# Optimization experiments

Hardware: AMD Instinct MI355X
Metric: run time of the kernel (lower is better)

## Reference

```python
import jax, jax.numpy as jnp
import numpy as np

N_NODES = 50000
N_EDGES = 1000000
D = 64          # input feature dim
H = 64          # hidden dim per conv layer / pooling out dim
N_GRAPHS = 256  # number of graphs in the batch


def setup_inputs() -> dict:
    key = jax.random.key(0)
    ks = jax.random.split(key, 10)
    x = jax.random.normal(ks[0], (N_NODES, D), dtype=jnp.float32)
    edge_index = jax.random.randint(ks[1], (2, N_EDGES), 0, N_NODES, dtype=jnp.int64)
    batch = jnp.sort(jax.random.randint(ks[2], (N_NODES,), 0, N_GRAPHS, dtype=jnp.int64))
    scale_in = 1.0 / np.sqrt(D)
    scale_h = 1.0 / np.sqrt(H)
    W1 = jax.random.normal(ks[3], (D, H), dtype=jnp.float32) * scale_in
    W2 = jax.random.normal(ks[4], (H, H), dtype=jnp.float32) * scale_h
    W3 = jax.random.normal(ks[5], (H, H), dtype=jnp.float32) * scale_h
    Wp1 = jax.random.normal(ks[6], (H, H), dtype=jnp.float32) * scale_h
    Wp2 = jax.random.normal(ks[7], (H, H), dtype=jnp.float32) * scale_h
    Wp3 = jax.random.normal(ks[8], (H, H), dtype=jnp.float32) * scale_h
    return {"x": x, "edge_index": edge_index, "batch": batch,
            "W1": W1, "W2": W2, "W3": W3,
            "Wp1": Wp1, "Wp2": Wp2, "Wp3": Wp3}


def _gcn_conv(x, W, src, dst):
    # PyG GCNConv with normalize=False, bias=False:
    #   h = x @ W; out[i] = sum_{(j->i) in E} h[j]   (no self-loops, unit edge weight)
    h = x @ W                                   # [N, H]
    return jax.ops.segment_sum(h[src], dst, num_segments=N_NODES)  # [N, H]


def reference(x, edge_index, batch, W1, W2, W3, Wp1, Wp2, Wp3):
    src, dst = edge_index[0], edge_index[1]
    x1 = jax.nn.relu(_gcn_conv(x, W1, src, dst))    # layer 0 output
    x2 = jax.nn.relu(_gcn_conv(x1, W2, src, dst))   # layer 1 output
    x3 = jax.nn.relu(_gcn_conv(x2, W3, src, dst))   # layer 2 output
    # Pooling: global_add_pool per layer output -> per-layer Linear -> stack -> sum -> relu
    p1 = jax.ops.segment_sum(x1, batch, num_segments=N_GRAPHS) @ Wp1  # [G, H]
    p2 = jax.ops.segment_sum(x2, batch, num_segments=N_GRAPHS) @ Wp2
    p3 = jax.ops.segment_sum(x3, batch, num_segments=N_GRAPHS) @ Wp3
    return jax.nn.relu(p1 + p2 + p3)                # [G, H]
```

## Files before the change

kernel.cpp:

```cpp
#include <hip/hip_runtime.h>
#include <hip/hip_bf16.h>

#define NN 50000
#define NE 1000000
#define DIM 64
#define NG 256
#define NBUCK 196
#define ROUND 4096
#define NBLK 245
#define TOT2D (NBUCK * NBLK)
#define SCANB 47

__global__ __launch_bounds__(512) void hist2d_kernel(const int* __restrict__ dst,
                                                     int* __restrict__ hist) {
    __shared__ int h[NBUCK];
    int t = threadIdx.x;
    if (t < NBUCK) h[t] = 0;
    __syncthreads();
    int base = blockIdx.x * ROUND;
#pragma unroll
    for (int it = 0; it < 8; ++it) {
        int e = base + it * 512 + t;
        if (e < NE) atomicAdd(&h[dst[e] >> 8], 1);
    }
    __syncthreads();
    if (t < NBUCK) hist[t * NBLK + blockIdx.x] = h[t];
}

__global__ __launch_bounds__(1024) void scanA_kernel(const int* __restrict__ hist,
                                                     int* __restrict__ blocksum) {
    __shared__ int tmp[1024];
    int t = threadIdx.x;
    int i = blockIdx.x * 1024 + t;
    tmp[t] = (i < TOT2D) ? hist[i] : 0;
    __syncthreads();
    for (int s = 512; s > 0; s >>= 1) {
        if (t < s) tmp[t] += tmp[t + s];
        __syncthreads();
    }
    if (t == 0) blocksum[blockIdx.x] = tmp[0];
}

__global__ __launch_bounds__(64) void scanB_kernel(int* __restrict__ blocksum) {
    __shared__ int tmp[64];
    int t = threadIdx.x;
    int v = (t < SCANB) ? blocksum[t] : 0;
    tmp[t] = v;
    __syncthreads();
    for (int off = 1; off < 64; off <<= 1) {
        int a = (t >= off) ? tmp[t - off] : 0;
        __syncthreads();
        tmp[t] += a;
        __syncthreads();
    }
    if (t < SCANB) blocksum[t] = tmp[t] - v;
}

__global__ __launch_bounds__(1024) void scanC_kernel(const int* __restrict__ hist,
                                                     const int* __restrict__ blocksum,
                                                     int* __restrict__ scanned) {
    __shared__ int tmp[1024];
    int t = threadIdx.x;
    int i = blockIdx.x * 1024 + t;
    int v = (i < TOT2D) ? hist[i] : 0;
    tmp[t] = v;
    __syncthreads();
    for (int off = 1; off < 1024; off <<= 1) {
        int a = (t >= off) ? tmp[t - off] : 0;
        __syncthreads();
        tmp[t] += a;
        __syncthreads();
    }
    if (i < TOT2D) scanned[i] = tmp[t] - v + blocksum[blockIdx.x];
}

__global__ __launch_bounds__(512) void permute_kernel(
    const int* __restrict__ src, const int* __restrict__ dst,
    const int* __restrict__ scanned, unsigned int* __restrict__ bucketed) {
    __shared__ int cur[NBUCK];
    int t = threadIdx.x;
    int blk = blockIdx.x;
    if (t < NBUCK) cur[t] = scanned[t * NBLK + blk];
    __syncthreads();
    int base = blk * ROUND;
#pragma unroll
    for (int it = 0; it < 8; ++it) {
        int e = base + it * 512 + t;
        if (e < NE) {
            int d = dst[e];
            int s = src[e];
            int b = d >> 8;
            int pos = atomicAdd(&cur[b], 1);
            bucketed[pos] = ((unsigned int)(d & 255) << 16) | (unsigned int)s;
        }
    }
}

__global__ __launch_bounds__(512) void bucket_sort_kernel(
    const unsigned int* __restrict__ bucketed, const int* __restrict__ scanned,
    int* __restrict__ offsets, int* __restrict__ csr) {
    __shared__ int hist[256];
    __shared__ int sc[256];
    __shared__ int cur[256];
    int b = blockIdx.x;
    int t = threadIdx.x;
    if (t < 256) hist[t] = 0;
    __syncthreads();
    int gbase = scanned[b * NBLK];
    int gend  = (b < NBUCK - 1) ? scanned[(b + 1) * NBLK] : NE;
    int count = gend - gbase;
    const unsigned int* bd = bucketed + gbase;
    for (int e = t; e < count; e += 512) atomicAdd(&hist[bd[e] >> 16], 1);
    __syncthreads();
    if (t < 256) sc[t] = hist[t];
    __syncthreads();
    for (int off = 1; off < 256; off <<= 1) {
        int a = 0;
        if (t < 256 && t >= off) a = sc[t - off];
        __syncthreads();
        if (t < 256) sc[t] += a;
        __syncthreads();
    }
    if (t < 256) {
        int excl = sc[t] - hist[t];
        cur[t] = excl;
        int node = b * 256 + t;
        if (node < NN) offsets[node] = gbase + excl;
    }
    if (b == NBUCK - 1 && t == 0) offsets[NN] = NE;
    __syncthreads();
    for (int e = t; e < count; e += 512) {
        unsigned int v = bd[e];
        int p = atomicAdd(&cur[v >> 16], 1);
        csr[gbase + p] = (int)(v & 0xFFFFu);
    }
}

__global__ __launch_bounds__(128) void gemm64_kernel(const float* __restrict__ X,
                                                     const float* __restrict__ W,
                                                     float* __restrict__ H, int nrows) {
    __shared__ float Xl[128 * 65];
    int t = threadIdx.x;
    int base = blockIdx.x * 128;
    for (int idx = t; idx < 128 * 16; idx += 128) {
        int row = idx >> 4;
        int c4  = idx & 15;
        float4 v = make_float4(0.f, 0.f, 0.f, 0.f);
        if (base + row < nrows)
            v = *reinterpret_cast<const float4*>(&X[(size_t)(base + row) * 64 + c4 * 4]);
        float* p = &Xl[row * 65 + c4 * 4];
        p[0] = v.x; p[1] = v.y; p[2] = v.z; p[3] = v.w;
    }
    __syncthreads();
    float acc[64];
#pragma unroll
    for (int c = 0; c < 64; ++c) acc[c] = 0.f;
#pragma unroll 4
    for (int k = 0; k < 64; ++k) {
        float xv = Xl[t * 65 + k];
#pragma unroll
        for (int c4 = 0; c4 < 16; ++c4) {
            float4 w = *reinterpret_cast<const float4*>(&W[k * 64 + c4 * 4]);
            acc[c4 * 4 + 0] = fmaf(xv, w.x, acc[c4 * 4 + 0]);
            acc[c4 * 4 + 1] = fmaf(xv, w.y, acc[c4 * 4 + 1]);
            acc[c4 * 4 + 2] = fmaf(xv, w.z, acc[c4 * 4 + 2]);
            acc[c4 * 4 + 3] = fmaf(xv, w.w, acc[c4 * 4 + 3]);
        }
    }
    int row = base + t;
    if (row < nrows) {
#pragma unroll
        for (int c4 = 0; c4 < 16; ++c4) {
            float4 o = make_float4(acc[c4 * 4 + 0], acc[c4 * 4 + 1],
                                   acc[c4 * 4 + 2], acc[c4 * 4 + 3]);
            *reinterpret_cast<float4*>(&H[(size_t)row * 64 + c4 * 4]) = o;
        }
    }
}

__global__ void gather_kernel(const float* __restrict__ H, const int* __restrict__ offsets,
                              const int* __restrict__ csr, const int* __restrict__ batch,
                              float* __restrict__ Xout, float* __restrict__ pool) {
    int tid = blockIdx.x * blockDim.x + threadIdx.x;
    int lane = tid & 63;
    int gw = tid >> 6;
    int nw = (gridDim.x * blockDim.x) >> 6;
    for (int n = gw; n < NN; n += nw) {
        int beg = offsets[n], end = offsets[n + 1];
        float a0 = 0.f, a1 = 0.f, a2 = 0.f, a3 = 0.f;
        int i = beg;
        for (; i + 4 <= end; i += 4) {
            int s0 = csr[i], s1 = csr[i + 1], s2 = csr[i + 2], s3 = csr[i + 3];
            a0 += H[(size_t)s0 * 64 + lane];
            a1 += H[(size_t)s1 * 64 + lane];
            a2 += H[(size_t)s2 * 64 + lane];
            a3 += H[(size_t)s3 * 64 + lane];
        }
        for (; i < end; ++i) a0 += H[(size_t)csr[i] * 64 + lane];
        float v = fmaxf((a0 + a1) + (a2 + a3), 0.f);
        Xout[(size_t)n * 64 + lane] = v;
        unsafeAtomicAdd(&pool[(size_t)batch[n] * 64 + lane], v);
    }
}

__global__ void final_kernel(const float* __restrict__ P1, const float* __restrict__ P2,
                             const float* __restrict__ P3,
                             const float* __restrict__ Wp1, const float* __restrict__ Wp2,
                             const float* __restrict__ Wp3, float* __restrict__ out) {
    int g = blockIdx.x;
    int c = threadIdx.x;
    float acc = 0.f;
#pragma unroll
    for (int k = 0; k < 64; ++k) {
        acc = fmaf(P1[g * 64 + k], Wp1[k * 64 + c], acc);
        acc = fmaf(P2[g * 64 + k], Wp2[k * 64 + c], acc);
        acc = fmaf(P3[g * 64 + k], Wp3[k * 64 + c], acc);
    }
    out[g * 64 + c] = fmaxf(acc, 0.f);
}

extern "C" void kernel_launch(void* const* d_in, const int* in_sizes, int n_in,
                              void* d_out, int out_size, void* d_ws, size_t ws_size,
                              hipStream_t stream) {
    const float* x     = (const float*)d_in[0];
    const int*   eidx  = (const int*)d_in[1];
    const int*   batch = (const int*)d_in[2];
    const float* W1  = (const float*)d_in[3];
    const float* W2  = (const float*)d_in[4];
    const float* W3  = (const float*)d_in[5];
    const float* Wp1 = (const float*)d_in[6];
    const float* Wp2 = (const float*)d_in[7];
    const float* Wp3 = (const float*)d_in[8];
    float* out = (float*)d_out;

    const int* src = eidx;
    const int* dst = eidx + NE;

    float* bufA  = (float*)d_ws;
    float* bufB  = bufA + (size_t)NN * DIM;
    float* pool1 = bufB + (size_t)NN * DIM;
    float* pool2 = pool1 + (size_t)NG * DIM;
    float* pool3 = pool2 + (size_t)NG * DIM;
    int* hist     = (int*)(pool3 + (size_t)NG * DIM);
    int* scanned  = hist + TOT2D;
    int* blocksum = scanned + TOT2D;
    int* offsets  = blocksum + 64;
    unsigned int* bucketed = (unsigned int*)(offsets + NN + 1);
    int* csr      = (int*)(bucketed + NE);

    hipMemsetAsync(pool1, 0, (size_t)3 * NG * DIM * sizeof(float), stream);

    hist2d_kernel<<<NBLK, 512, 0, stream>>>(dst, hist);
    scanA_kernel<<<SCANB, 1024, 0, stream>>>(hist, blocksum);
    scanB_kernel<<<1, 64, 0, stream>>>(blocksum);
    scanC_kernel<<<SCANB, 1024, 0, stream>>>(hist, blocksum, scanned);
    permute_kernel<<<NBLK, 512, 0, stream>>>(src, dst, scanned, bucketed);
    bucket_sort_kernel<<<NBUCK, 512, 0, stream>>>(bucketed, scanned, offsets, csr);

    const int gemm_blocks = (NN + 127) / 128;
    const int gath_blocks = 2048;

    const float* xin = x;
    const float* Ws[3]   = {W1, W2, W3};
    float* pools[3] = {pool1, pool2, pool3};
    for (int l = 0; l < 3; ++l) {
        gemm64_kernel<<<gemm_blocks, 128, 0, stream>>>(xin, Ws[l], bufA, NN);
        gather_kernel<<<gath_blocks, 256, 0, stream>>>(bufA, offsets, csr, batch, bufB, pools[l]);
        xin = bufB;
    }
    final_kernel<<<NG, 64, 0, stream>>>(pool1, pool2, pool3, Wp1, Wp2, Wp3, out);
}
```

Baseline: 352.2 us.

## Store projected features in bf16, batch pool atomics, skip final layer X write

The GEMM output H is now stored as bf16, which halves the bytes fetched by the random-access edge gather. Each GEMM thread now computes half a row, and the block grows to 256 threads. The gather kernel gives each wave a contiguous chunk of nodes and accumulates pool sums locally, issuing an atomic only when the graph id changes, which cuts atomic traffic. The third layer no longer writes its unused node features. The bf16 intermediates lose precision in the aggregated features.

Result: slower. 418.1 us (+18.7%).

```diff
diff --git a/kernel.cpp b/kernel.cpp
--- a/kernel.cpp
+++ b/kernel.cpp
@@ -136,13 +136,14 @@
     }
 }
 
-__global__ __launch_bounds__(128) void gemm64_kernel(const float* __restrict__ X,
+__global__ __launch_bounds__(256) void gemm64_kernel(const float* __restrict__ X,
                                                      const float* __restrict__ W,
-                                                     float* __restrict__ H, int nrows) {
+                                                     __hip_bfloat16* __restrict__ H,
+                                                     int nrows) {
     __shared__ float Xl[128 * 65];
     int t = threadIdx.x;
     int base = blockIdx.x * 128;
-    for (int idx = t; idx < 128 * 16; idx += 128) {
+    for (int idx = t; idx < 128 * 16; idx += 256) {
         int row = idx >> 4;
         int c4  = idx & 15;
         float4 v = make_float4(0.f, 0.f, 0.f, 0.f);
@@ -152,55 +153,72 @@
         p[0] = v.x; p[1] = v.y; p[2] = v.z; p[3] = v.w;
     }
     __syncthreads();
-    float acc[64];
-#pragma unroll
-    for (int c = 0; c < 64; ++c) acc[c] = 0.f;
+    int r    = t >> 1;
+    int half = t & 1;
+    float acc[32];
+#pragma unroll
+    for (int c = 0; c < 32; ++c) acc[c] = 0.f;
 #pragma unroll 4
     for (int k = 0; k < 64; ++k) {
-        float xv = Xl[t * 65 + k];
-#pragma unroll
-        for (int c4 = 0; c4 < 16; ++c4) {
-            float4 w = *reinterpret_cast<const float4*>(&W[k * 64 + c4 * 4]);
+        float xv = Xl[r * 65 + k];
+#pragma unroll
+        for (int c4 = 0; c4 < 8; ++c4) {
+            float4 w = *reinterpret_cast<const float4*>(&W[k * 64 + half * 32 + c4 * 4]);
             acc[c4 * 4 + 0] = fmaf(xv, w.x, acc[c4 * 4 + 0]);
             acc[c4 * 4 + 1] = fmaf(xv, w.y, acc[c4 * 4 + 1]);
             acc[c4 * 4 + 2] = fmaf(xv, w.z, acc[c4 * 4 + 2]);
             acc[c4 * 4 + 3] = fmaf(xv, w.w, acc[c4 * 4 + 3]);
         }
     }
-    int row = base + t;
+    int row = base + r;
     if (row < nrows) {
-#pragma unroll
-        for (int c4 = 0; c4 < 16; ++c4) {
-            float4 o = make_float4(acc[c4 * 4 + 0], acc[c4 * 4 + 1],
-                                   acc[c4 * 4 + 2], acc[c4 * 4 + 3]);
-            *reinterpret_cast<float4*>(&H[(size_t)row * 64 + c4 * 4]) = o;
-        }
-    }
-}
-
-__global__ void gather_kernel(const float* __restrict__ H, const int* __restrict__ offsets,
+        alignas(16) __hip_bfloat16 hb[32];
+#pragma unroll
+        for (int c = 0; c < 32; ++c) hb[c] = __float2bfloat16(acc[c]);
+        uint4* dst4 = reinterpret_cast<uint4*>(&H[(size_t)row * 64 + half * 32]);
+        const uint4* src4 = reinterpret_cast<const uint4*>(hb);
+#pragma unroll
+        for (int q = 0; q < 4; ++q) dst4[q] = src4[q];
+    }
+}
+
+template <bool WRITE_X>
+__global__ void gather_kernel(const __hip_bfloat16* __restrict__ H,
+                              const int* __restrict__ offsets,
                               const int* __restrict__ csr, const int* __restrict__ batch,
                               float* __restrict__ Xout, float* __restrict__ pool) {
     int tid = blockIdx.x * blockDim.x + threadIdx.x;
     int lane = tid & 63;
     int gw = tid >> 6;
     int nw = (gridDim.x * blockDim.x) >> 6;
-    for (int n = gw; n < NN; n += nw) {
+    int chunk = (NN + nw - 1) / nw;
+    int start = gw * chunk;
+    if (start >= NN) return;
+    int stop = min(start + chunk, NN);
+    float pacc = 0.f;
+    int curg = batch[start];
+    for (int n = start; n < stop; ++n) {
         int beg = offsets[n], end = offsets[n + 1];
         float a0 = 0.f, a1 = 0.f, a2 = 0.f, a3 = 0.f;
         int i = beg;
         for (; i + 4 <= end; i += 4) {
             int s0 = csr[i], s1 = csr[i + 1], s2 = csr[i + 2], s3 = csr[i + 3];
-            a0 += H[(size_t)s0 * 64 + lane];
-            a1 += H[(size_t)s1 * 64 + lane];
-            a2 += H[(size_t)s2 * 64 + lane];
-            a3 += H[(size_t)s3 * 64 + lane];
-        }
-        for (; i < end; ++i) a0 += H[(size_t)csr[i] * 64 + lane];
+            a0 += __bfloat162float(H[(size_t)s0 * 64 + lane]);
+            a1 += __bfloat162float(H[(size_t)s1 * 64 + lane]);
+            a2 += __bfloat162float(H[(size_t)s2 * 64 + lane]);
+            a3 += __bfloat162float(H[(size_t)s3 * 64 + lane]);
+        }
+        for (; i < end; ++i) a0 += __bfloat162float(H[(size_t)csr[i] * 64 + lane]);
         float v = fmaxf((a0 + a1) + (a2 + a3), 0.f);
-        Xout[(size_t)n * 64 + lane] = v;
-        unsafeAtomicAdd(&pool[(size_t)batch[n] * 64 + lane], v);
-    }
+        if (WRITE_X) Xout[(size_t)n * 64 + lane] = v;
+        int g = batch[n];
+        if (g != curg) {
+            unsafeAtomicAdd(&pool[(size_t)curg * 64 + lane], pacc);
+            pacc = 0.f; curg = g;
+        }
+        pacc += v;
+    }
+    unsafeAtomicAdd(&pool[(size_t)curg * 64 + lane], pacc);
 }
 
 __global__ void final_kernel(const float* __restrict__ P1, const float* __restrict__ P2,
@@ -236,9 +254,9 @@
     const int* src = eidx;
     const int* dst = eidx + NE;
 
-    float* bufA  = (float*)d_ws;
-    float* bufB  = bufA + (size_t)NN * DIM;
-    float* pool1 = bufB + (size_t)NN * DIM;
+    __hip_bfloat16* bufH = (__hip_bfloat16*)d_ws;
+    float* bufX  = (float*)(bufH + (size_t)NN * DIM);
+    float* pool1 = bufX + (size_t)NN * DIM;
     float* pool2 = pool1 + (size_t)NG * DIM;
     float* pool3 = pool2 + (size_t)NG * DIM;
     int* hist     = (int*)(pool3 + (size_t)NG * DIM);
@@ -260,13 +278,12 @@
     const int gemm_blocks = (NN + 127) / 128;
     const int gath_blocks = 2048;
 
-    const float* xin = x;
-    const float* Ws[3]   = {W1, W2, W3};
-    float* pools[3] = {pool1, pool2, pool3};
-    for (int l = 0; l < 3; ++l) {
-        gemm64_kernel<<<gemm_blocks, 128, 0, stream>>>(xin, Ws[l], bufA, NN);
-        gather_kernel<<<gath_blocks, 256, 0, stream>>>(bufA, offsets, csr, batch, bufB, pools[l]);
-        xin = bufB;
-    }
+    gemm64_kernel<<<gemm_blocks, 256, 0, stream>>>(x, W1, bufH, NN);
+    gather_kernel<true><<<gath_blocks, 256, 0, stream>>>(bufH, offsets, csr, batch, bufX, pool1);
+    gemm64_kernel<<<gemm_blocks, 256, 0, stream>>>(bufX, W2, bufH, NN);
+    gather_kernel<true><<<gath_blocks, 256, 0, stream>>>(bufH, offsets, csr, batch, bufX, pool2);
+    gemm64_kernel<<<gemm_blocks, 256, 0, stream>>>(bufX, W3, bufH, NN);
+    gather_kernel<false><<<gath_blocks, 256, 0, stream>>>(bufH, offsets, csr, batch, nullptr, pool3);
+
     final_kernel<<<NG, 64, 0, stream>>>(pool1, pool2, pool3, Wp1, Wp2, Wp3, out);
 }
```
